# Optimization experiments

Hardware: AMD Instinct MI355X
Metric: run time of the kernel (lower is better)

Reference implementation:

```python
import jax, jax.numpy as jnp
import numpy as np

L, C, K, V, G, T, NC, CIN = 9, 256, 3, 25, 9, 128, 60, 3


def _ln(x, w, b, axes, eps=1e-5):
    # LayerNorm over (channels, joints) per time step, affine params broadcast over time
    m = x.mean(axes, keepdims=True)
    v = x.var(axes, keepdims=True)
    return (x - m) * jax.lax.rsqrt(v + eps) * w + b


def setup_inputs() -> dict:
    key = jax.random.key(0)
    ks = jax.random.split(key, 8)
    s = 0.02  # weight init scale
    return {
        "x": jax.random.normal(ks[0], (1, CIN, T, V), jnp.float32),
        "A": jax.random.uniform(ks[1], (K, V, V), jnp.float32),
        "ln_in_w": jnp.ones((CIN, V), jnp.float32),
        "ln_in_b": jnp.zeros((CIN, V), jnp.float32),
        "W_in": jax.random.normal(ks[2], (C, CIN), jnp.float32) * s,
        "b_in": jnp.zeros((C,), jnp.float32),
        "Wg": jax.random.normal(ks[3], (L, K * C, C), jnp.float32) * s,
        "bg": jnp.zeros((L, K * C), jnp.float32),
        "ln1_w": jnp.ones((L, C, V), jnp.float32),
        "ln1_b": jnp.zeros((L, C, V), jnp.float32),
        "Wt": jax.random.normal(ks[4], (L, C, C, G), jnp.float32) * s,
        "bt": jnp.zeros((L, C), jnp.float32),
        "ln2_w": jnp.ones((L, C, V), jnp.float32),
        "ln2_b": jnp.zeros((L, C, V), jnp.float32),
        "imp": jnp.ones((L, K, V, V), jnp.float32),
        "W_out": jax.random.normal(ks[5], (NC, C), jnp.float32) * s,
        "b_out": jnp.zeros((NC,), jnp.float32),
    }


def reference(x, A, ln_in_w, ln_in_b, W_in, b_in, Wg, bg, ln1_w, ln1_b,
              Wt, bt, ln2_w, ln2_b, imp, W_out, b_out):
    ghalf = G // 2
    Al = A[None] * imp                      # (L, K, V, V) edge-importance weighted adjacency
    xs = x[0].transpose(1, 0, 2)            # (T, CIN, V): stream frames
    fifo0 = jnp.zeros((L, C, G, V), x.dtype)

    def step(carry, xt):
        fifo, fifo_res = carry
        # input LayerNorm + 1x1 conv (fcn_in)
        h = _ln(xt, ln_in_w, ln_in_b, (0, 1))
        h = jnp.einsum('oc,cv->ov', W_in, h) + b_in[:, None]   # (C, V)
        new_f, new_fr = [], []
        for l in range(L):
            res = h                                             # identity residual (in==out, stride==1)
            # graph conv: 1x1 conv -> (K, C, V), einsum with partitioned adjacency
            y = (jnp.einsum('oc,cv->ov', Wg[l], h) + bg[l][:, None]).reshape(K, C, V)
            z = jnp.einsum('kcv,kvw->cw', y, Al[l])             # (C, V)
            # FIFO shift: newest frame at time index 0
            f = jnp.concatenate([z[:, None, :], fifo[l, :, :-1]], axis=1)      # (C, G, V)
            fr = jnp.concatenate([res[:, None, :], fifo_res[l, :, :-1]], axis=1)
            # tcn: LN -> ReLU -> temporal conv (G,1) -> LN
            a = jax.nn.relu(_ln(f, ln1_w[l][:, None, :], ln1_b[l][:, None, :], (0, 2)))
            t = jnp.einsum('ocg,cgv->ov', Wt[l], a) + bt[l][:, None]           # (C, V)
            t = _ln(t, ln2_w[l], ln2_b[l], (0, 1))
            # residual from center of residual FIFO, then ReLU
            h = jax.nn.relu(t + fr[:, ghalf])
            new_f.append(f)
            new_fr.append(fr)
        pooled = h.mean(axis=1)                                 # avg_pool2d over (T=1, V)
        logits = W_out @ pooled + b_out                         # (NC,)
        return (jnp.stack(new_f), jnp.stack(new_fr)), logits

    _, out = jax.lax.scan(step, (fifo0, fifo0), xs)
    return out  # (T, NC): per-frame class logits
```

## Files before the change

### kernel.cpp

```cpp
#include <hip/hip_runtime.h>

#define TT  128
#define CC  256
#define VV  25
#define KK  3
#define GG  9
#define LL  9
#define NCC 60
#define CINN 3
#define TV    (TT*VV)
#define N4    4096
#define KDIM2 (CC*GG)
#define UR    ((TT+8)*32)
#define YSTR  104
#define HSTR  264

typedef __attribute__((ext_vector_type(8))) short bf16x8;
typedef __attribute__((ext_vector_type(4))) float f32x4;
typedef unsigned short us16;

__device__ __forceinline__ us16 f2bf(float f) {
    union { float f; unsigned u; } a; a.f = f;
    unsigned r = a.u + 0x7fff + ((a.u >> 16) & 1);
    return (us16)(r >> 16);
}
__device__ __forceinline__ float bf2f(us16 u) {
    union { unsigned u; float f; } a; a.u = ((unsigned)u) << 16; return a.f;
}
__device__ __forceinline__ bf16x8 ld8(const us16* p) { return *(const bf16x8*)p; }


#define PN1 (LL*KK*CC*CC)
#define PN2 (LL*CC*CC*GG)
#define PN3 (LL*KK*32*32)
#define PN4 (LL*CC*32)
#define PTOT (PN1+PN2+PN3+PN4)

__global__ void k_prep(const float* __restrict__ Wg, const float* __restrict__ Wt,
                       const float* __restrict__ A, const float* __restrict__ imp,
                       const float* __restrict__ bg,
                       us16* __restrict__ Wgb, us16* __restrict__ Wt2b,
                       us16* __restrict__ AlTb, float* __restrict__ bgAl) {
    int i = blockIdx.x * 256 + threadIdx.x;
    if (i < PN1) {
        Wgb[i] = f2bf(Wg[i]);
    } else if (i < PN1 + PN2) {
        int j = i - PN1;
        int kk = j % (CC*GG);
        int o  = (j / (CC*GG)) % CC;
        int l  = j / (CC*CC*GG);
        int g = kk >> 8, c = kk & 255;
        Wt2b[j] = f2bf(Wt[((size_t)(l*CC + o)*CC + c)*GG + g]);
    } else if (i < PN1 + PN2 + PN3) {
        int j = i - PN1 - PN2;
        int v = j & 31, w = (j >> 5) & 31;
        int lk = j >> 10, k = lk % KK, l = lk / KK;
        float val = 0.f;
        if (v < VV && w < VV)
            val = A[(k*VV+v)*VV + w] * imp[((size_t)(l*KK+k)*VV+v)*VV + w];
        AlTb[j] = f2bf(val);
    } else if (i < PTOT) {
        int j = i - PN1 - PN2 - PN3;
        int w = j & 31, c = (j >> 5) & 255, l = j >> 13;
        float s = 0.f;
        if (w < VV) {
            for (int k = 0; k < KK; k++) {
                float col = 0.f;
                for (int v = 0; v < VV; v++)
                    col += A[(k*VV+v)*VV + w] * imp[((size_t)(l*KK+k)*VV+v)*VV + w];
                s += bg[l*KK*CC + k*CC + c] * col;
            }
        }
        bgAl[j] = s;
    }
}


__device__ __forceinline__ void blk_reduce2(float& s, float& q, float* red) {
    #pragma unroll
    for (int off = 32; off; off >>= 1) {
        s += __shfl_down(s, off);
        q += __shfl_down(q, off);
    }
    int lane = threadIdx.x & 63, w = threadIdx.x >> 6;
    if (lane == 0) { red[w] = s; red[4+w] = q; }
    __syncthreads();
    s = red[0]+red[1]+red[2]+red[3];
    q = red[4]+red[5]+red[6]+red[7];
}


template<int FIRST>
__global__ __launch_bounds__(256, 1) void k_gcn(
    const float* __restrict__ x, const float* __restrict__ lniw,
    const float* __restrict__ lnib, const float* __restrict__ Win,
    const float* __restrict__ bin,
    const us16* __restrict__ Tt, const float* __restrict__ btv,
    const float* __restrict__ ln2w, const float* __restrict__ ln2b,
    const us16* __restrict__ HresidTb,
    const us16* __restrict__ Wgb,
    const us16* __restrict__ AlTb, const float* __restrict__ bgAl,
    const float* __restrict__ lnw, const float* __restrict__ lnb,
    us16* __restrict__ HTb, us16* __restrict__ Ut2) {

    const int t = blockIdx.x, tid = threadIdx.x;
    if (t >= TT) {
        int tp = t - TT, c = tid;
        #pragma unroll
        for (int w = 0; w < 32; w++) {
            float u = (w < VV) ? fmaxf(lnb[c*VV + w], 0.f) : 0.f;
            Ut2[(size_t)(tp*32 + w)*CC + c] = f2bf(u);
        }
        return;
    }
    __shared__ __align__(16) us16 Yt[CC*YSTR];
    __shared__ __align__(16) us16 sH[32*HSTR];
    __shared__ float red[8];
    __shared__ float sx[80];
    __shared__ float sh[80];
    const int wave = tid >> 6, lane = tid & 63, quad = lane >> 4, l16 = lane & 15;

    if (FIRST) {
        if (tid < CINN*VV)
            sx[tid] = x[(size_t)(tid/VV)*TV + t*VV + (tid%VV)];
        __syncthreads();
        float s = 0.f, q = 0.f;
        for (int i = 0; i < CINN*VV; i++) { float v = sx[i]; s += v; q += v*v; }
        float m  = s * (1.f/75.f);
        float var = q * (1.f/75.f) - m*m;
        float rs = rsqrtf(var + 1e-5f);
        if (tid < CINN*VV)
            sh[tid] = (sx[tid]-m)*rs*lniw[tid] + lnib[tid];
        __syncthreads();
        int c = tid;
        float w0 = Win[c*3+0], w1 = Win[c*3+1], w2 = Win[c*3+2], bb = bin[c];
        #pragma unroll
        for (int v = 0; v < VV; v++) {
            float acc = bb + w0*sh[v] + w1*sh[VV+v] + w2*sh[2*VV+v];
            us16 b = f2bf(acc);
            HTb[(size_t)(t*32 + v)*CC + c] = b;
            sH[v*HSTR + c] = b;
        }
        #pragma unroll
        for (int v = VV; v < 32; v++)
            sH[v*HSTR + c] = 0;
        __syncthreads();
    } else {
        int c = tid;
        float btc = btv[c];
        float vals[VV];
        float s = 0.f, q = 0.f;
        #pragma unroll
        for (int v = 0; v < VV; v++) {
            float xv = bf2f(Tt[(size_t)(t*32 + v)*CC + c]) + btc;
            vals[v] = xv; s += xv; q += xv*xv;
        }
        blk_reduce2(s, q, red);
        float m = s * (1.f/6400.f);
        float var = q * (1.f/6400.f) - m*m;
        float rs = rsqrtf(var + 1e-5f);
        #pragma unroll
        for (int v = 0; v < VV; v++) {
            float res = (t >= 4) ? bf2f(HresidTb[(size_t)((t-4)*32 + v)*CC + c]) : 0.f;
            float o = fmaxf((vals[v]-m)*rs*ln2w[c*VV+v] + ln2b[c*VV+v] + res, 0.f);
            us16 b = f2bf(o);
            HTb[(size_t)(t*32 + v)*CC + c] = b;
            sH[v*HSTR + c] = b;
        }
        #pragma unroll
        for (int v = VV; v < 32; v++)
            sH[v*HSTR + c] = 0;
        __syncthreads();
    }

    bf16x8 al[2][3];
    #pragma unroll
    for (int nt = 0; nt < 2; nt++)
        #pragma unroll
        for (int s = 0; s < 3; s++)
            al[nt][s] = ld8(AlTb + (size_t)(s*32 + nt*16 + l16)*32 + quad*8);

    bf16x8 bf[2][8];
    #pragma unroll
    for (int nt = 0; nt < 2; nt++)
        #pragma unroll
        for (int s = 0; s < 8; s++)
            bf[nt][s] = *(const bf16x8*)(sH + (nt*16 + l16)*HSTR + s*32 + quad*8);

    bf16x8 wA0,wA1,wA2,wA3,wA4,wA5,wA6,wA7;
    bf16x8 wB0,wB1,wB2,wB3,wB4,wB5,wB6,wB7;
    bf16x8 wC0,wC1,wC2,wC3,wC4,wC5,wC6,wC7;

#define PLD(S, mtv) { \
    const us16* ap_ = Wgb + (size_t)(wave*192 + (mtv)*16 + l16)*CC + quad*8; \
    S##0 = ld8(ap_);       S##1 = ld8(ap_ + 32); \
    S##2 = ld8(ap_ + 64);  S##3 = ld8(ap_ + 96); \
    S##4 = ld8(ap_ + 128); S##5 = ld8(ap_ + 160); \
    S##6 = ld8(ap_ + 192); S##7 = ld8(ap_ + 224); }
#define PMFW(S, mtv) { \
    f32x4 p0a = {}, p0b = {}, p1a = {}, p1b = {}; \
    p0a = __builtin_amdgcn_mfma_f32_16x16x32_bf16(S##0, bf[0][0], p0a,0,0,0); \
    p1a = __builtin_amdgcn_mfma_f32_16x16x32_bf16(S##0, bf[1][0], p1a,0,0,0); \
    p0b = __builtin_amdgcn_mfma_f32_16x16x32_bf16(S##1, bf[0][1], p0b,0,0,0); \
    p1b = __builtin_amdgcn_mfma_f32_16x16x32_bf16(S##1, bf[1][1], p1b,0,0,0); \
    p0a = __builtin_amdgcn_mfma_f32_16x16x32_bf16(S##2, bf[0][2], p0a,0,0,0); \
    p1a = __builtin_amdgcn_mfma_f32_16x16x32_bf16(S##2, bf[1][2], p1a,0,0,0); \
    p0b = __builtin_amdgcn_mfma_f32_16x16x32_bf16(S##3, bf[0][3], p0b,0,0,0); \
    p1b = __builtin_amdgcn_mfma_f32_16x16x32_bf16(S##3, bf[1][3], p1b,0,0,0); \
    p0a = __builtin_amdgcn_mfma_f32_16x16x32_bf16(S##4, bf[0][4], p0a,0,0,0); \
    p1a = __builtin_amdgcn_mfma_f32_16x16x32_bf16(S##4, bf[1][4], p1a,0,0,0); \
    p0b = __builtin_amdgcn_mfma_f32_16x16x32_bf16(S##5, bf[0][5], p0b,0,0,0); \
    p1b = __builtin_amdgcn_mfma_f32_16x16x32_bf16(S##5, bf[1][5], p1b,0,0,0); \
    p0a = __builtin_amdgcn_mfma_f32_16x16x32_bf16(S##6, bf[0][6], p0a,0,0,0); \
    p1a = __builtin_amdgcn_mfma_f32_16x16x32_bf16(S##6, bf[1][6], p1a,0,0,0); \
    p0b = __builtin_amdgcn_mfma_f32_16x16x32_bf16(S##7, bf[0][7], p0b,0,0,0); \
    p1b = __builtin_amdgcn_mfma_f32_16x16x32_bf16(S##7, bf[1][7], p1b,0,0,0); \
    int mb_ = wave*192 + (mtv)*16 + quad*4; \
    _Pragma("unroll") \
    for (int r_ = 0; r_ < 4; r_++) { \
        int m_ = mb_ + r_; \
        int base_ = (m_ & 255)*YSTR + (m_ >> 8)*32 + l16; \
        Yt[base_]      = f2bf(p0a[r_] + p0b[r_]); \
        Yt[base_ + 16] = f2bf(p1a[r_] + p1b[r_]); \
    } }

    PLD(wA, 0); PLD(wB, 1); PLD(wC, 2);
    #pragma unroll 1
    for (int mt = 0; mt < 9; mt += 3) {
        PMFW(wA, mt);     PLD(wA, mt + 3);
        PMFW(wB, mt + 1); PLD(wB, mt + 4);
        PMFW(wC, mt + 2); PLD(wC, mt + 5);
    }
    PMFW(wA, 9); PMFW(wB, 10); PMFW(wC, 11);
#undef PLD
#undef PMFW
    __syncthreads();

    f32x4 z[4][2];
    #pragma unroll
    for (int mt = 0; mt < 4; mt++) { z[mt][0] = (f32x4){}; z[mt][1] = (f32x4){}; }
    #pragma unroll
    for (int mt = 0; mt < 4; mt++)
        #pragma unroll
        for (int s = 0; s < 3; s++) {
            bf16x8 a = *(const bf16x8*)(Yt + (wave*64 + mt*16 + l16)*YSTR + s*32 + quad*8);
            z[mt][0] = __builtin_amdgcn_mfma_f32_16x16x32_bf16(a, al[0][s], z[mt][0], 0,0,0);
            z[mt][1] = __builtin_amdgcn_mfma_f32_16x16x32_bf16(a, al[1][s], z[mt][1], 0,0,0);
        }

    float s_ = 0.f, q_ = 0.f;
    #pragma unroll
    for (int mt = 0; mt < 4; mt++)
        #pragma unroll
        for (int nt = 0; nt < 2; nt++)
            #pragma unroll
            for (int r = 0; r < 4; r++) {
                int c = wave*64 + mt*16 + quad*4 + r;
                int w = nt*16 + l16;
                float zb = z[mt][nt][r] + bgAl[c*32 + w];
                z[mt][nt][r] = zb;
                if (w < VV) { s_ += zb; q_ += zb*zb; }
            }
    blk_reduce2(s_, q_, red);
    float m = s_ * (1.f/6400.f);
    float var = q_ * (1.f/6400.f) - m*m;
    float rs = rsqrtf(var + 1e-5f);
    #pragma unroll
    for (int mt = 0; mt < 4; mt++)
        #pragma unroll
        for (int nt = 0; nt < 2; nt++) {
            int w = nt*16 + l16;
            if (w < VV) {
                int c0 = wave*64 + mt*16 + quad*4;
                ushort4 pk;
                float u0 = fmaxf((z[mt][nt][0]-m)*rs*lnw[(c0+0)*VV+w] + lnb[(c0+0)*VV+w], 0.f);
                float u1 = fmaxf((z[mt][nt][1]-m)*rs*lnw[(c0+1)*VV+w] + lnb[(c0+1)*VV+w], 0.f);
                float u2 = fmaxf((z[mt][nt][2]-m)*rs*lnw[(c0+2)*VV+w] + lnb[(c0+2)*VV+w], 0.f);
                float u3 = fmaxf((z[mt][nt][3]-m)*rs*lnw[(c0+3)*VV+w] + lnb[(c0+3)*VV+w], 0.f);
                pk.x = f2bf(u0); pk.y = f2bf(u1); pk.z = f2bf(u2); pk.w = f2bf(u3);
                *(ushort4*)(Ut2 + (size_t)((t+8)*32 + w)*CC + c0) = pk;
            }
        }
    #pragma unroll
    for (int r = VV; r < 32; r++)
        Ut2[(size_t)((t+8)*32 + r)*CC + tid] = 0;
}


__global__ __launch_bounds__(256) void k_gemm2(const us16* __restrict__ A,
                                               const us16* __restrict__ Ut2,
                                               us16* __restrict__ Tt) {
    __shared__ us16 TL[64*72];
    const int tid = threadIdx.x;
    const int wave = tid >> 6, lane = tid & 63, quad = lane >> 4, l16 = lane & 15;
    const int bid = blockIdx.x;
    const int xcd = bid & 7, grp = bid >> 3;
    const int mt = (xcd >> 2)*2 + (grp & 1);
    const int nt = (xcd & 3)*16 + (grp >> 1);
    const int m0b = mt*64, n0b = nt*64;
    const int m0w = m0b + (wave & 1)*32;
    const int n0w = n0b + (wave >> 1)*32;
    const us16* ap = A + (size_t)(m0w + l16)*KDIM2 + quad*8;
    f32x4 acc00 = {}, acc01 = {}, acc10 = {}, acc11 = {};
    bf16x8 aA0,aA1,bA0,bA1, aB0,aB1,bB0,bB1, aC0,aC1,bC0,bC1, aD0,aD1,bD0,bD1;

#define GLD(S, it) { \
    int k0 = (it)*32; \
    a##S##0 = ld8(ap + k0); \
    a##S##1 = ld8(ap + k0 + 16*KDIM2); \
    int g = k0 >> 8; \
    const us16* bp = Ut2 + (size_t)(n0w + (8-g)*32 + l16)*CC + (k0 & 255) + quad*8; \
    b##S##0 = ld8(bp); \
    b##S##1 = ld8(bp + 16*CC); }
#define GMF(S) { \
    acc00 = __builtin_amdgcn_mfma_f32_16x16x32_bf16(a##S##0, b##S##0, acc00,0,0,0); \
    acc01 = __builtin_amdgcn_mfma_f32_16x16x32_bf16(a##S##0, b##S##1, acc01,0,0,0); \
    acc10 = __builtin_amdgcn_mfma_f32_16x16x32_bf16(a##S##1, b##S##0, acc10,0,0,0); \
    acc11 = __builtin_amdgcn_mfma_f32_16x16x32_bf16(a##S##1, b##S##1, acc11,0,0,0); }

    GLD(A, 0); GLD(B, 1); GLD(C, 2); GLD(D, 3);
    #pragma unroll 1
    for (int it = 4; it <= KDIM2/32 - 4; it += 4) {
        GMF(A); GLD(A, it);
        GMF(B); GLD(B, it+1);
        GMF(C); GLD(C, it+2);
        GMF(D); GLD(D, it+3);
    }
    GMF(A); GMF(B); GMF(C); GMF(D);
#undef GLD
#undef GMF

    #pragma unroll
    for (int r = 0; r < 4; r++) {
        int mlo = (wave & 1)*32 + quad*4 + r;
        int nlo = (wave >> 1)*32 + l16;
        TL[nlo*72 + mlo]           = f2bf(acc00[r]);
        TL[(nlo+16)*72 + mlo]      = f2bf(acc01[r]);
        TL[nlo*72 + mlo + 16]      = f2bf(acc10[r]);
        TL[(nlo+16)*72 + mlo + 16] = f2bf(acc11[r]);
    }
    __syncthreads();
    #pragma unroll
    for (int u = 0; u < 2; u++) {
        int q2 = tid + u*256;
        int row = q2 >> 3, ch = q2 & 7;
        *(bf16x8*)(Tt + (size_t)(n0b + row)*CC + m0b + ch*8) =
            *(const bf16x8*)(TL + row*72 + ch*8);
    }
}


__global__ __launch_bounds__(256) void k_fin(const us16* __restrict__ Tt,
                                             const us16* __restrict__ HresidTb,
                                             const float* __restrict__ btv,
                                             const float* __restrict__ lnw,
                                             const float* __restrict__ lnb,
                                             const float* __restrict__ Wout,
                                             const float* __restrict__ bout,
                                             float* __restrict__ out) {
    int t = blockIdx.x, tid = threadIdx.x;
    __shared__ float red[8];
    __shared__ float sp[CC];
    int c = tid;
    float btc = btv[c];
    float vals[VV];
    float s = 0.f, q = 0.f;
    #pragma unroll
    for (int v = 0; v < VV; v++) {
        float xv = bf2f(Tt[(size_t)(t*32 + v)*CC + c]) + btc;
        vals[v] = xv; s += xv; q += xv*xv;
    }
    blk_reduce2(s, q, red);
    float m = s * (1.f/6400.f);
    float var = q * (1.f/6400.f) - m*m;
    float rs = rsqrtf(var + 1e-5f);
    float pl = 0.f;
    #pragma unroll
    for (int v = 0; v < VV; v++) {
        float res = (t >= 4) ? bf2f(HresidTb[(size_t)((t-4)*32 + v)*CC + c]) : 0.f;
        float o = fmaxf((vals[v]-m)*rs*lnw[c*VV+v] + lnb[c*VV+v] + res, 0.f);
        pl += o;
    }
    sp[c] = pl * (1.f/VV);
    __syncthreads();
    if (tid < NCC) {
        float a = bout[tid];
        for (int cc = 0; cc < CC; cc++) a = fmaf(Wout[tid*CC+cc], sp[cc], a);
        out[t*NCC + tid] = a;
    }
}


extern "C" void kernel_launch(void* const* d_in, const int* in_sizes, int n_in,
                              void* d_out, int out_size, void* d_ws, size_t ws_size,
                              hipStream_t stream) {
    const float* x    = (const float*)d_in[0];
    const float* A    = (const float*)d_in[1];
    const float* lniw = (const float*)d_in[2];
    const float* lnib = (const float*)d_in[3];
    const float* Win  = (const float*)d_in[4];
    const float* bin  = (const float*)d_in[5];
    const float* Wg   = (const float*)d_in[6];
    const float* bg   = (const float*)d_in[7];
    const float* ln1w = (const float*)d_in[8];
    const float* ln1b = (const float*)d_in[9];
    const float* Wt   = (const float*)d_in[10];
    const float* bt   = (const float*)d_in[11];
    const float* ln2w = (const float*)d_in[12];
    const float* ln2b = (const float*)d_in[13];
    const float* imp  = (const float*)d_in[14];
    const float* Wout = (const float*)d_in[15];
    const float* bout = (const float*)d_in[16];
    float* out = (float*)d_out;

    float* ws = (float*)d_ws;
    size_t off = 0;
    auto alloc = [&](size_t n) { float* p = ws + off; off += (n + 255) & ~(size_t)255; return p; };
    float* bgAl = alloc((size_t)LL*CC*32);
    us16* HTb0 = (us16*)alloc((size_t)TT*32*CC/2);
    us16* HTb1 = (us16*)alloc((size_t)TT*32*CC/2);
    us16* Tt   = (us16*)alloc((size_t)N4*CC/2);
    us16* Wgb  = (us16*)alloc((size_t)LL*KK*CC*CC/2);
    us16* Wt2b = (us16*)alloc((size_t)LL*CC*KDIM2/2);
    us16* Ut2  = (us16*)alloc((size_t)UR*CC/2);
    us16* AlTb = (us16*)alloc((size_t)LL*KK*32*32/2);
    (void)ws_size; (void)in_sizes; (void)n_in; (void)out_size;

    k_prep<<<(PTOT + 255)/256, 256, 0, stream>>>(Wg, Wt, A, imp, bg,
                                                 Wgb, Wt2b, AlTb, bgAl);

    us16* hPrev = HTb0; us16* hNext = HTb1;
    for (int l = 0; l < LL; l++) {
        if (l == 0) {
            k_gcn<1><<<TT + 8, 256, 0, stream>>>(
                x, lniw, lnib, Win, bin,
                Tt, bt, ln2w, ln2b, hPrev,
                Wgb, AlTb, bgAl, ln1w, ln1b,
                hPrev , Ut2);
        } else {
            k_gcn<0><<<TT + 8, 256, 0, stream>>>(
                x, lniw, lnib, Win, bin,
                Tt, bt + (size_t)(l-1)*CC,
                ln2w + (size_t)(l-1)*CC*VV, ln2b + (size_t)(l-1)*CC*VV,
                hPrev ,
                Wgb + (size_t)l*KK*CC*CC,
                AlTb + (size_t)l*KK*32*32, bgAl + (size_t)l*CC*32,
                ln1w + (size_t)l*CC*VV, ln1b + (size_t)l*CC*VV,
                hNext , Ut2);
            us16* tmp = hPrev; hPrev = hNext; hNext = tmp;
        }
        k_gemm2<<<256, 256, 0, stream>>>(
            Wt2b + (size_t)l*CC*KDIM2, Ut2, Tt);
    }
    k_fin<<<TT, 256, 0, stream>>>(Tt, hPrev,
        bt + (size_t)(LL-1)*CC, ln2w + (size_t)(LL-1)*CC*VV, ln2b + (size_t)(LL-1)*CC*VV,
        Wout, bout, out);
}
```

Measured before the change: 712.5 us.

## Split temporal-conv GEMM K dimension in two with fp32 partial outputs

The temporal-conv GEMM is split along its K dimension (2304) into two halves of 36 iterations each, doubling the grid from 256 to 512 blocks. Each half writes fp32 partial sums to its own buffer, and the consumer kernels (k_gcn and k_fin) add the two partials when they read them. The aim is better occupancy of the GPU's compute units with twice as many blocks, each running a shorter K loop. In exchange, the intermediate buffer grows fourfold (two fp32 copies instead of one bf16 copy), which adds write and read traffic, and each block's pipeline prologue and epilogue is amortised over fewer iterations.

```diff
diff --git a/kernel.cpp b/kernel.cpp
--- a/kernel.cpp
+++ b/kernel.cpp
@@ -95,7 +95,7 @@
     const float* __restrict__ x, const float* __restrict__ lniw,
     const float* __restrict__ lnib, const float* __restrict__ Win,
     const float* __restrict__ bin,
-    const us16* __restrict__ Tt, const float* __restrict__ btv,
+    const float* __restrict__ Tp, const float* __restrict__ btv,
     const float* __restrict__ ln2w, const float* __restrict__ ln2b,
     const us16* __restrict__ HresidTb,
     const us16* __restrict__ Wgb,
@@ -152,7 +152,8 @@
         float s = 0.f, q = 0.f;
         #pragma unroll
         for (int v = 0; v < VV; v++) {
-            float xv = bf2f(Tt[(size_t)(t*32 + v)*CC + c]) + btc;
+            size_t idx = (size_t)(t*32 + v)*CC + c;
+            float xv = Tp[idx] + Tp[(size_t)N4*CC + idx] + btc;
             vals[v] = xv; s += xv; q += xv*xv;
         }
         blk_reduce2(s, q, red);
@@ -289,17 +290,19 @@
 
 __global__ __launch_bounds__(256) void k_gemm2(const us16* __restrict__ A,
                                                const us16* __restrict__ Ut2,
-                                               us16* __restrict__ Tt) {
-    __shared__ us16 TL[64*72];
+                                               float* __restrict__ Tp) {
+    __shared__ __align__(16) float TLf[64*72];
     const int tid = threadIdx.x;
     const int wave = tid >> 6, lane = tid & 63, quad = lane >> 4, l16 = lane & 15;
     const int bid = blockIdx.x;
-    const int xcd = bid & 7, grp = bid >> 3;
+    const int inner = bid & 255, ks = bid >> 8;
+    const int xcd = inner & 7, grp = inner >> 3;
     const int mt = (xcd >> 2)*2 + (grp & 1);
     const int nt = (xcd & 3)*16 + (grp >> 1);
     const int m0b = mt*64, n0b = nt*64;
     const int m0w = m0b + (wave & 1)*32;
     const int n0w = n0b + (wave >> 1)*32;
+    const int it0 = ks*36;
     const us16* ap = A + (size_t)(m0w + l16)*KDIM2 + quad*8;
     f32x4 acc00 = {}, acc01 = {}, acc10 = {}, acc11 = {};
     bf16x8 aA0,aA1,bA0,bA1, aB0,aB1,bB0,bB1, aC0,aC1,bC0,bC1, aD0,aD1,bD0,bD1;
@@ -318,9 +321,9 @@
     acc10 = __builtin_amdgcn_mfma_f32_16x16x32_bf16(a##S##1, b##S##0, acc10,0,0,0); \
     acc11 = __builtin_amdgcn_mfma_f32_16x16x32_bf16(a##S##1, b##S##1, acc11,0,0,0); }
 
-    GLD(A, 0); GLD(B, 1); GLD(C, 2); GLD(D, 3);
+    GLD(A, it0); GLD(B, it0+1); GLD(C, it0+2); GLD(D, it0+3);
     #pragma unroll 1
-    for (int it = 4; it <= KDIM2/32 - 4; it += 4) {
+    for (int it = it0 + 4; it <= it0 + 36 - 4; it += 4) {
         GMF(A); GLD(A, it);
         GMF(B); GLD(B, it+1);
         GMF(C); GLD(C, it+2);
@@ -334,23 +337,24 @@
     for (int r = 0; r < 4; r++) {
         int mlo = (wave & 1)*32 + quad*4 + r;
         int nlo = (wave >> 1)*32 + l16;
-        TL[nlo*72 + mlo]           = f2bf(acc00[r]);
-        TL[(nlo+16)*72 + mlo]      = f2bf(acc01[r]);
-        TL[nlo*72 + mlo + 16]      = f2bf(acc10[r]);
-        TL[(nlo+16)*72 + mlo + 16] = f2bf(acc11[r]);
+        TLf[nlo*72 + mlo]           = acc00[r];
+        TLf[(nlo+16)*72 + mlo]      = acc01[r];
+        TLf[nlo*72 + mlo + 16]      = acc10[r];
+        TLf[(nlo+16)*72 + mlo + 16] = acc11[r];
     }
     __syncthreads();
-    #pragma unroll
-    for (int u = 0; u < 2; u++) {
+    float* dst = Tp + (size_t)ks*N4*CC;
+    #pragma unroll
+    for (int u = 0; u < 4; u++) {
         int q2 = tid + u*256;
-        int row = q2 >> 3, ch = q2 & 7;
-        *(bf16x8*)(Tt + (size_t)(n0b + row)*CC + m0b + ch*8) =
-            *(const bf16x8*)(TL + row*72 + ch*8);
-    }
-}
-
-
-__global__ __launch_bounds__(256) void k_fin(const us16* __restrict__ Tt,
+        int row = q2 >> 4, ch = q2 & 15;
+        *(float4*)(dst + (size_t)(n0b + row)*CC + m0b + ch*4) =
+            *(const float4*)(TLf + row*72 + ch*4);
+    }
+}
+
+
+__global__ __launch_bounds__(256) void k_fin(const float* __restrict__ Tp,
                                              const us16* __restrict__ HresidTb,
                                              const float* __restrict__ btv,
                                              const float* __restrict__ lnw,
@@ -367,7 +371,8 @@
     float s = 0.f, q = 0.f;
     #pragma unroll
     for (int v = 0; v < VV; v++) {
-        float xv = bf2f(Tt[(size_t)(t*32 + v)*CC + c]) + btc;
+        size_t idx = (size_t)(t*32 + v)*CC + c;
+        float xv = Tp[idx] + Tp[(size_t)N4*CC + idx] + btc;
         vals[v] = xv; s += xv; q += xv*xv;
     }
     blk_reduce2(s, q, red);
@@ -419,7 +424,7 @@
     float* bgAl = alloc((size_t)LL*CC*32);
     us16* HTb0 = (us16*)alloc((size_t)TT*32*CC/2);
     us16* HTb1 = (us16*)alloc((size_t)TT*32*CC/2);
-    us16* Tt   = (us16*)alloc((size_t)N4*CC/2);
+    float* Tp  = alloc((size_t)2*N4*CC);
     us16* Wgb  = (us16*)alloc((size_t)LL*KK*CC*CC/2);
     us16* Wt2b = (us16*)alloc((size_t)LL*CC*KDIM2/2);
     us16* Ut2  = (us16*)alloc((size_t)UR*CC/2);
@@ -434,13 +439,13 @@
         if (l == 0) {
             k_gcn<1><<<TT + 8, 256, 0, stream>>>(
                 x, lniw, lnib, Win, bin,
-                Tt, bt, ln2w, ln2b, hPrev,
+                Tp, bt, ln2w, ln2b, hPrev,
                 Wgb, AlTb, bgAl, ln1w, ln1b,
                 hPrev , Ut2);
         } else {
             k_gcn<0><<<TT + 8, 256, 0, stream>>>(
                 x, lniw, lnib, Win, bin,
-                Tt, bt + (size_t)(l-1)*CC,
+                Tp, bt + (size_t)(l-1)*CC,
                 ln2w + (size_t)(l-1)*CC*VV, ln2b + (size_t)(l-1)*CC*VV,
                 hPrev ,
                 Wgb + (size_t)l*KK*CC*CC,
@@ -449,10 +454,10 @@
                 hNext , Ut2);
             us16* tmp = hPrev; hPrev = hNext; hNext = tmp;
         }
-        k_gemm2<<<256, 256, 0, stream>>>(
-            Wt2b + (size_t)l*CC*KDIM2, Ut2, Tt);
-    }
-    k_fin<<<TT, 256, 0, stream>>>(Tt, hPrev,
+        k_gemm2<<<512, 256, 0, stream>>>(
+            Wt2b + (size_t)l*CC*KDIM2, Ut2, Tp);
+    }
+    k_fin<<<TT, 256, 0, stream>>>(Tp, hPrev,
         bt + (size_t)(LL-1)*CC, ln2w + (size_t)(LL-1)*CC*VV, ln2b + (size_t)(LL-1)*CC*VV,
         Wout, bout, out);
 }
```

After: 734.3 us. 1.03x slower.

## Fuse per-layer kernels into one persistent kernel with grid barriers

Applied to the files above, without the earlier changes.

Replaces the 19 separate launches (graph-conv kernel and temporal GEMM per layer, plus the final head) with one persistent 256-block kernel. Stages are separated by a software grid barrier built on device-scope atomics, and the barrier counter is zeroed in the prep kernel. This removes launch overhead and the gaps between kernels. In exchange, all 256 blocks must be co-resident, the barrier spin costs time, and the ping-pong pointer swap happens before the barrier. Register and LDS pressure also rise, since both stages now share one kernel.

```diff
diff --git a/kernel.cpp b/kernel.cpp
--- a/kernel.cpp
+++ b/kernel.cpp
@@ -14,6 +14,7 @@
 #define UR    ((TT+8)*32)
 #define YSTR  104
 #define HSTR  264
+#define GRID  256
 
 typedef __attribute__((ext_vector_type(8))) short bf16x8;
 typedef __attribute__((ext_vector_type(4))) float f32x4;
@@ -28,6 +29,25 @@
     union { unsigned u; float f; } a; a.u = ((unsigned)u) << 16; return a.f;
 }
 __device__ __forceinline__ bf16x8 ld8(const us16* p) { return *(const bf16x8*)p; }
+
+
+__device__ __forceinline__ void gbar(unsigned* bar) {
+    __syncthreads();
+    if (threadIdx.x == 0) {
+        __threadfence();
+        unsigned g = __hip_atomic_load(bar + 1, __ATOMIC_RELAXED, __HIP_MEMORY_SCOPE_AGENT);
+        unsigned a = __hip_atomic_fetch_add(bar, 1u, __ATOMIC_ACQ_REL, __HIP_MEMORY_SCOPE_AGENT);
+        if (a == GRID - 1) {
+            __hip_atomic_store(bar, 0u, __ATOMIC_RELAXED, __HIP_MEMORY_SCOPE_AGENT);
+            __hip_atomic_store(bar + 1, g + 1u, __ATOMIC_RELEASE, __HIP_MEMORY_SCOPE_AGENT);
+        } else {
+            while (__hip_atomic_load(bar + 1, __ATOMIC_ACQUIRE, __HIP_MEMORY_SCOPE_AGENT) == g)
+                __builtin_amdgcn_s_sleep(2);
+        }
+        __threadfence();
+    }
+    __syncthreads();
+}
 
 
 #define PN1 (LL*KK*CC*CC)
@@ -40,8 +60,10 @@
                        const float* __restrict__ A, const float* __restrict__ imp,
                        const float* __restrict__ bg,
                        us16* __restrict__ Wgb, us16* __restrict__ Wt2b,
-                       us16* __restrict__ AlTb, float* __restrict__ bgAl) {
+                       us16* __restrict__ AlTb, float* __restrict__ bgAl,
+                       unsigned* __restrict__ bar) {
     int i = blockIdx.x * 256 + threadIdx.x;
+    if (i < 8) bar[i] = 0u;
     if (i < PN1) {
         Wgb[i] = f2bf(Wg[i]);
     } else if (i < PN1 + PN2) {
@@ -90,109 +112,124 @@
 }
 
 
-template<int FIRST>
-__global__ __launch_bounds__(256, 1) void k_gcn(
-    const float* __restrict__ x, const float* __restrict__ lniw,
-    const float* __restrict__ lnib, const float* __restrict__ Win,
-    const float* __restrict__ bin,
-    const us16* __restrict__ Tt, const float* __restrict__ btv,
-    const float* __restrict__ ln2w, const float* __restrict__ ln2b,
-    const us16* __restrict__ HresidTb,
-    const us16* __restrict__ Wgb,
-    const us16* __restrict__ AlTb, const float* __restrict__ bgAl,
-    const float* __restrict__ lnw, const float* __restrict__ lnb,
-    us16* __restrict__ HTb, us16* __restrict__ Ut2) {
-
-    const int t = blockIdx.x, tid = threadIdx.x;
-    if (t >= TT) {
-        int tp = t - TT, c = tid;
-        #pragma unroll
-        for (int w = 0; w < 32; w++) {
-            float u = (w < VV) ? fmaxf(lnb[c*VV + w], 0.f) : 0.f;
-            Ut2[(size_t)(tp*32 + w)*CC + c] = f2bf(u);
-        }
-        return;
-    }
+struct FA {
+    const float *x, *lniw, *lnib, *Win, *bin;
+    const float *bt, *ln2w, *ln2b;
+    const float *ln1w, *ln1b;
+    const us16  *Wgb, *AlTb, *Wt2b;
+    const float *bgAl;
+    const float *Wout, *bout;
+    us16 *HTb0, *HTb1, *Tt, *Ut2;
+    unsigned *bar;
+    float *out;
+};
+
+__global__ __launch_bounds__(256, 1) void k_fused(FA a) {
+    const int bid = blockIdx.x, tid = threadIdx.x;
     __shared__ __align__(16) us16 Yt[CC*YSTR];
     __shared__ __align__(16) us16 sH[32*HSTR];
     __shared__ float red[8];
     __shared__ float sx[80];
     __shared__ float sh[80];
     const int wave = tid >> 6, lane = tid & 63, quad = lane >> 4, l16 = lane & 15;
-
-    if (FIRST) {
-        if (tid < CINN*VV)
-            sx[tid] = x[(size_t)(tid/VV)*TV + t*VV + (tid%VV)];
-        __syncthreads();
-        float s = 0.f, q = 0.f;
-        for (int i = 0; i < CINN*VV; i++) { float v = sx[i]; s += v; q += v*v; }
-        float m  = s * (1.f/75.f);
-        float var = q * (1.f/75.f) - m*m;
-        float rs = rsqrtf(var + 1e-5f);
-        if (tid < CINN*VV)
-            sh[tid] = (sx[tid]-m)*rs*lniw[tid] + lnib[tid];
-        __syncthreads();
-        int c = tid;
-        float w0 = Win[c*3+0], w1 = Win[c*3+1], w2 = Win[c*3+2], bb = bin[c];
-        #pragma unroll
-        for (int v = 0; v < VV; v++) {
-            float acc = bb + w0*sh[v] + w1*sh[VV+v] + w2*sh[2*VV+v];
-            us16 b = f2bf(acc);
-            HTb[(size_t)(t*32 + v)*CC + c] = b;
-            sH[v*HSTR + c] = b;
-        }
-        #pragma unroll
-        for (int v = VV; v < 32; v++)
-            sH[v*HSTR + c] = 0;
-        __syncthreads();
-    } else {
-        int c = tid;
-        float btc = btv[c];
-        float vals[VV];
-        float s = 0.f, q = 0.f;
-        #pragma unroll
-        for (int v = 0; v < VV; v++) {
-            float xv = bf2f(Tt[(size_t)(t*32 + v)*CC + c]) + btc;
-            vals[v] = xv; s += xv; q += xv*xv;
-        }
-        blk_reduce2(s, q, red);
-        float m = s * (1.f/6400.f);
-        float var = q * (1.f/6400.f) - m*m;
-        float rs = rsqrtf(var + 1e-5f);
-        #pragma unroll
-        for (int v = 0; v < VV; v++) {
-            float res = (t >= 4) ? bf2f(HresidTb[(size_t)((t-4)*32 + v)*CC + c]) : 0.f;
-            float o = fmaxf((vals[v]-m)*rs*ln2w[c*VV+v] + ln2b[c*VV+v] + res, 0.f);
-            us16 b = f2bf(o);
-            HTb[(size_t)(t*32 + v)*CC + c] = b;
-            sH[v*HSTR + c] = b;
-        }
-        #pragma unroll
-        for (int v = VV; v < 32; v++)
-            sH[v*HSTR + c] = 0;
-        __syncthreads();
-    }
-
-    bf16x8 al[2][3];
-    #pragma unroll
-    for (int nt = 0; nt < 2; nt++)
-        #pragma unroll
-        for (int s = 0; s < 3; s++)
-            al[nt][s] = ld8(AlTb + (size_t)(s*32 + nt*16 + l16)*32 + quad*8);
-
-    bf16x8 bf[2][8];
-    #pragma unroll
-    for (int nt = 0; nt < 2; nt++)
-        #pragma unroll
-        for (int s = 0; s < 8; s++)
-            bf[nt][s] = *(const bf16x8*)(sH + (nt*16 + l16)*HSTR + s*32 + quad*8);
-
-    bf16x8 wA0,wA1,wA2,wA3,wA4,wA5,wA6,wA7;
-    bf16x8 wB0,wB1,wB2,wB3,wB4,wB5,wB6,wB7;
-    bf16x8 wC0,wC1,wC2,wC3,wC4,wC5,wC6,wC7;
+    const int t = bid;
+
+    us16* hPrev = a.HTb0;
+    us16* hNext = a.HTb1;
+
+    #pragma unroll 1
+    for (int l = 0; l < LL; l++) {
+        const us16*  WgbL  = a.Wgb  + (size_t)l*KK*CC*CC;
+        const us16*  AlTbL = a.AlTb + (size_t)l*KK*32*32;
+        const float* bgAlL = a.bgAl + (size_t)l*CC*32;
+        const float* lnwL  = a.ln1w + (size_t)l*CC*VV;
+        const float* lnbL  = a.ln1b + (size_t)l*CC*VV;
+        us16* Hout = (l == 0) ? hPrev : hNext;
+
+        if (t >= TT && t < TT + 8) {
+            int tp = t - TT, c = tid;
+            #pragma unroll
+            for (int w = 0; w < 32; w++) {
+                float u = (w < VV) ? fmaxf(lnbL[c*VV + w], 0.f) : 0.f;
+                a.Ut2[(size_t)(tp*32 + w)*CC + c] = f2bf(u);
+            }
+        } else if (t < TT) {
+            if (l == 0) {
+                if (tid < CINN*VV)
+                    sx[tid] = a.x[(size_t)(tid/VV)*TV + t*VV + (tid%VV)];
+                __syncthreads();
+                float s = 0.f, q = 0.f;
+                for (int i = 0; i < CINN*VV; i++) { float v = sx[i]; s += v; q += v*v; }
+                float m  = s * (1.f/75.f);
+                float var = q * (1.f/75.f) - m*m;
+                float rs = rsqrtf(var + 1e-5f);
+                if (tid < CINN*VV)
+                    sh[tid] = (sx[tid]-m)*rs*a.lniw[tid] + a.lnib[tid];
+                __syncthreads();
+                int c = tid;
+                float w0 = a.Win[c*3+0], w1 = a.Win[c*3+1], w2 = a.Win[c*3+2], bb = a.bin[c];
+                #pragma unroll
+                for (int v = 0; v < VV; v++) {
+                    float acc = bb + w0*sh[v] + w1*sh[VV+v] + w2*sh[2*VV+v];
+                    us16 b = f2bf(acc);
+                    Hout[(size_t)(t*32 + v)*CC + c] = b;
+                    sH[v*HSTR + c] = b;
+                }
+                #pragma unroll
+                for (int v = VV; v < 32; v++)
+                    sH[v*HSTR + c] = 0;
+                __syncthreads();
+            } else {
+                const float* btv = a.bt   + (size_t)(l-1)*CC;
+                const float* l2w = a.ln2w + (size_t)(l-1)*CC*VV;
+                const float* l2b = a.ln2b + (size_t)(l-1)*CC*VV;
+                int c = tid;
+                float btc = btv[c];
+                float vals[VV];
+                float s = 0.f, q = 0.f;
+                #pragma unroll
+                for (int v = 0; v < VV; v++) {
+                    float xv = bf2f(a.Tt[(size_t)(t*32 + v)*CC + c]) + btc;
+                    vals[v] = xv; s += xv; q += xv*xv;
+                }
+                blk_reduce2(s, q, red);
+                float m = s * (1.f/6400.f);
+                float var = q * (1.f/6400.f) - m*m;
+                float rs = rsqrtf(var + 1e-5f);
+                #pragma unroll
+                for (int v = 0; v < VV; v++) {
+                    float res = (t >= 4) ? bf2f(hPrev[(size_t)((t-4)*32 + v)*CC + c]) : 0.f;
+                    float o = fmaxf((vals[v]-m)*rs*l2w[c*VV+v] + l2b[c*VV+v] + res, 0.f);
+                    us16 b = f2bf(o);
+                    Hout[(size_t)(t*32 + v)*CC + c] = b;
+                    sH[v*HSTR + c] = b;
+                }
+                #pragma unroll
+                for (int v = VV; v < 32; v++)
+                    sH[v*HSTR + c] = 0;
+                __syncthreads();
+            }
+
+            bf16x8 al[2][3];
+            #pragma unroll
+            for (int nt = 0; nt < 2; nt++)
+                #pragma unroll
+                for (int s = 0; s < 3; s++)
+                    al[nt][s] = ld8(AlTbL + (size_t)(s*32 + nt*16 + l16)*32 + quad*8);
+
+            bf16x8 bf[2][8];
+            #pragma unroll
+            for (int nt = 0; nt < 2; nt++)
+                #pragma unroll
+                for (int s = 0; s < 8; s++)
+                    bf[nt][s] = *(const bf16x8*)(sH + (nt*16 + l16)*HSTR + s*32 + quad*8);
+
+            bf16x8 wA0,wA1,wA2,wA3,wA4,wA5,wA6,wA7;
+            bf16x8 wB0,wB1,wB2,wB3,wB4,wB5,wB6,wB7;
+            bf16x8 wC0,wC1,wC2,wC3,wC4,wC5,wC6,wC7;
 
 #define PLD(S, mtv) { \
-    const us16* ap_ = Wgb + (size_t)(wave*192 + (mtv)*16 + l16)*CC + quad*8; \
+    const us16* ap_ = WgbL + (size_t)(wave*192 + (mtv)*16 + l16)*CC + quad*8; \
     S##0 = ld8(ap_);       S##1 = ld8(ap_ + 32); \
     S##2 = ld8(ap_ + 64);  S##3 = ld8(ap_ + 96); \
     S##4 = ld8(ap_ + 128); S##5 = ld8(ap_ + 160); \
@@ -224,92 +261,90 @@
         Yt[base_ + 16] = f2bf(p1a[r_] + p1b[r_]); \
     } }
 
-    PLD(wA, 0); PLD(wB, 1); PLD(wC, 2);
-    #pragma unroll 1
-    for (int mt = 0; mt < 9; mt += 3) {
-        PMFW(wA, mt);     PLD(wA, mt + 3);
-        PMFW(wB, mt + 1); PLD(wB, mt + 4);
-        PMFW(wC, mt + 2); PLD(wC, mt + 5);
-    }
-    PMFW(wA, 9); PMFW(wB, 10); PMFW(wC, 11);
+            PLD(wA, 0); PLD(wB, 1); PLD(wC, 2);
+            #pragma unroll 1
+            for (int mt = 0; mt < 9; mt += 3) {
+                PMFW(wA, mt);     PLD(wA, mt + 3);
+                PMFW(wB, mt + 1); PLD(wB, mt + 4);
+                PMFW(wC, mt + 2); PLD(wC, mt + 5);
+            }
+            PMFW(wA, 9); PMFW(wB, 10); PMFW(wC, 11);
 #undef PLD
 #undef PMFW
-    __syncthreads();
-
-    f32x4 z[4][2];
-    #pragma unroll
-    for (int mt = 0; mt < 4; mt++) { z[mt][0] = (f32x4){}; z[mt][1] = (f32x4){}; }
-    #pragma unroll
-    for (int mt = 0; mt < 4; mt++)
-        #pragma unroll
-        for (int s = 0; s < 3; s++) {
-            bf16x8 a = *(const bf16x8*)(Yt + (wave*64 + mt*16 + l16)*YSTR + s*32 + quad*8);
-            z[mt][0] = __builtin_amdgcn_mfma_f32_16x16x32_bf16(a, al[0][s], z[mt][0], 0,0,0);
-            z[mt][1] = __builtin_amdgcn_mfma_f32_16x16x32_bf16(a, al[1][s], z[mt][1], 0,0,0);
-        }
-
-    float s_ = 0.f, q_ = 0.f;
-    #pragma unroll
-    for (int mt = 0; mt < 4; mt++)
-        #pragma unroll
-        for (int nt = 0; nt < 2; nt++)
-            #pragma unroll
-            for (int r = 0; r < 4; r++) {
-                int c = wave*64 + mt*16 + quad*4 + r;
-                int w = nt*16 + l16;
-                float zb = z[mt][nt][r] + bgAl[c*32 + w];
-                z[mt][nt][r] = zb;
-                if (w < VV) { s_ += zb; q_ += zb*zb; }
-            }
-    blk_reduce2(s_, q_, red);
-    float m = s_ * (1.f/6400.f);
-    float var = q_ * (1.f/6400.f) - m*m;
-    float rs = rsqrtf(var + 1e-5f);
-    #pragma unroll
-    for (int mt = 0; mt < 4; mt++)
-        #pragma unroll
-        for (int nt = 0; nt < 2; nt++) {
-            int w = nt*16 + l16;
-            if (w < VV) {
-                int c0 = wave*64 + mt*16 + quad*4;
-                ushort4 pk;
-                float u0 = fmaxf((z[mt][nt][0]-m)*rs*lnw[(c0+0)*VV+w] + lnb[(c0+0)*VV+w], 0.f);
-                float u1 = fmaxf((z[mt][nt][1]-m)*rs*lnw[(c0+1)*VV+w] + lnb[(c0+1)*VV+w], 0.f);
-                float u2 = fmaxf((z[mt][nt][2]-m)*rs*lnw[(c0+2)*VV+w] + lnb[(c0+2)*VV+w], 0.f);
-                float u3 = fmaxf((z[mt][nt][3]-m)*rs*lnw[(c0+3)*VV+w] + lnb[(c0+3)*VV+w], 0.f);
-                pk.x = f2bf(u0); pk.y = f2bf(u1); pk.z = f2bf(u2); pk.w = f2bf(u3);
-                *(ushort4*)(Ut2 + (size_t)((t+8)*32 + w)*CC + c0) = pk;
-            }
-        }
-    #pragma unroll
-    for (int r = VV; r < 32; r++)
-        Ut2[(size_t)((t+8)*32 + r)*CC + tid] = 0;
-}
-
-
-__global__ __launch_bounds__(256) void k_gemm2(const us16* __restrict__ A,
-                                               const us16* __restrict__ Ut2,
-                                               us16* __restrict__ Tt) {
-    __shared__ us16 TL[64*72];
-    const int tid = threadIdx.x;
-    const int wave = tid >> 6, lane = tid & 63, quad = lane >> 4, l16 = lane & 15;
-    const int bid = blockIdx.x;
-    const int xcd = bid & 7, grp = bid >> 3;
-    const int mt = (xcd >> 2)*2 + (grp & 1);
-    const int nt = (xcd & 3)*16 + (grp >> 1);
-    const int m0b = mt*64, n0b = nt*64;
-    const int m0w = m0b + (wave & 1)*32;
-    const int n0w = n0b + (wave >> 1)*32;
-    const us16* ap = A + (size_t)(m0w + l16)*KDIM2 + quad*8;
-    f32x4 acc00 = {}, acc01 = {}, acc10 = {}, acc11 = {};
-    bf16x8 aA0,aA1,bA0,bA1, aB0,aB1,bB0,bB1, aC0,aC1,bC0,bC1, aD0,aD1,bD0,bD1;
+            __syncthreads();
+
+            f32x4 z[4][2];
+            #pragma unroll
+            for (int mt = 0; mt < 4; mt++) { z[mt][0] = (f32x4){}; z[mt][1] = (f32x4){}; }
+            #pragma unroll
+            for (int mt = 0; mt < 4; mt++)
+                #pragma unroll
+                for (int s = 0; s < 3; s++) {
+                    bf16x8 av = *(const bf16x8*)(Yt + (wave*64 + mt*16 + l16)*YSTR + s*32 + quad*8);
+                    z[mt][0] = __builtin_amdgcn_mfma_f32_16x16x32_bf16(av, al[0][s], z[mt][0], 0,0,0);
+                    z[mt][1] = __builtin_amdgcn_mfma_f32_16x16x32_bf16(av, al[1][s], z[mt][1], 0,0,0);
+                }
+
+            float s_ = 0.f, q_ = 0.f;
+            #pragma unroll
+            for (int mt = 0; mt < 4; mt++)
+                #pragma unroll
+                for (int nt = 0; nt < 2; nt++)
+                    #pragma unroll
+                    for (int r = 0; r < 4; r++) {
+                        int c = wave*64 + mt*16 + quad*4 + r;
+                        int w = nt*16 + l16;
+                        float zb = z[mt][nt][r] + bgAlL[c*32 + w];
+                        z[mt][nt][r] = zb;
+                        if (w < VV) { s_ += zb; q_ += zb*zb; }
+                    }
+            blk_reduce2(s_, q_, red);
+            float m = s_ * (1.f/6400.f);
+            float var = q_ * (1.f/6400.f) - m*m;
+            float rs = rsqrtf(var + 1e-5f);
+            #pragma unroll
+            for (int mt = 0; mt < 4; mt++)
+                #pragma unroll
+                for (int nt = 0; nt < 2; nt++) {
+                    int w = nt*16 + l16;
+                    if (w < VV) {
+                        int c0 = wave*64 + mt*16 + quad*4;
+                        ushort4 pk;
+                        float u0 = fmaxf((z[mt][nt][0]-m)*rs*lnwL[(c0+0)*VV+w] + lnbL[(c0+0)*VV+w], 0.f);
+                        float u1 = fmaxf((z[mt][nt][1]-m)*rs*lnwL[(c0+1)*VV+w] + lnbL[(c0+1)*VV+w], 0.f);
+                        float u2 = fmaxf((z[mt][nt][2]-m)*rs*lnwL[(c0+2)*VV+w] + lnbL[(c0+2)*VV+w], 0.f);
+                        float u3 = fmaxf((z[mt][nt][3]-m)*rs*lnwL[(c0+3)*VV+w] + lnbL[(c0+3)*VV+w], 0.f);
+                        pk.x = f2bf(u0); pk.y = f2bf(u1); pk.z = f2bf(u2); pk.w = f2bf(u3);
+                        *(ushort4*)(a.Ut2 + (size_t)((t+8)*32 + w)*CC + c0) = pk;
+                    }
+                }
+            #pragma unroll
+            for (int r = VV; r < 32; r++)
+                a.Ut2[(size_t)((t+8)*32 + r)*CC + tid] = 0;
+        }
+
+        if (l > 0) { us16* tmp = hPrev; hPrev = hNext; hNext = tmp; }
+        gbar(a.bar);
+
+        {
+            const us16* Awt = a.Wt2b + (size_t)l*CC*KDIM2;
+            us16* TL = Yt;
+            const int xcd = bid & 7, grp = bid >> 3;
+            const int mt = (xcd >> 2)*2 + (grp & 1);
+            const int nt = (xcd & 3)*16 + (grp >> 1);
+            const int m0b = mt*64, n0b = nt*64;
+            const int m0w = m0b + (wave & 1)*32;
+            const int n0w = n0b + (wave >> 1)*32;
+            const us16* ap = Awt + (size_t)(m0w + l16)*KDIM2 + quad*8;
+            f32x4 acc00 = {}, acc01 = {}, acc10 = {}, acc11 = {};
+            bf16x8 aA0,aA1,bA0,bA1, aB0,aB1,bB0,bB1, aC0,aC1,bC0,bC1, aD0,aD1,bD0,bD1;
 
 #define GLD(S, it) { \
     int k0 = (it)*32; \
     a##S##0 = ld8(ap + k0); \
     a##S##1 = ld8(ap + k0 + 16*KDIM2); \
     int g = k0 >> 8; \
-    const us16* bp = Ut2 + (size_t)(n0w + (8-g)*32 + l16)*CC + (k0 & 255) + quad*8; \
+    const us16* bp = a.Ut2 + (size_t)(n0w + (8-g)*32 + l16)*CC + (k0 & 255) + quad*8; \
     b##S##0 = ld8(bp); \
     b##S##1 = ld8(bp + 16*CC); }
 #define GMF(S) { \
@@ -318,75 +353,71 @@
     acc10 = __builtin_amdgcn_mfma_f32_16x16x32_bf16(a##S##1, b##S##0, acc10,0,0,0); \
     acc11 = __builtin_amdgcn_mfma_f32_16x16x32_bf16(a##S##1, b##S##1, acc11,0,0,0); }
 
-    GLD(A, 0); GLD(B, 1); GLD(C, 2); GLD(D, 3);
-    #pragma unroll 1
-    for (int it = 4; it <= KDIM2/32 - 4; it += 4) {
-        GMF(A); GLD(A, it);
-        GMF(B); GLD(B, it+1);
-        GMF(C); GLD(C, it+2);
-        GMF(D); GLD(D, it+3);
-    }
-    GMF(A); GMF(B); GMF(C); GMF(D);
+            GLD(A, 0); GLD(B, 1); GLD(C, 2); GLD(D, 3);
+            #pragma unroll 1
+            for (int it = 4; it <= KDIM2/32 - 4; it += 4) {
+                GMF(A); GLD(A, it);
+                GMF(B); GLD(B, it+1);
+                GMF(C); GLD(C, it+2);
+                GMF(D); GLD(D, it+3);
+            }
+            GMF(A); GMF(B); GMF(C); GMF(D);
 #undef GLD
 #undef GMF
 
-    #pragma unroll
-    for (int r = 0; r < 4; r++) {
-        int mlo = (wave & 1)*32 + quad*4 + r;
-        int nlo = (wave >> 1)*32 + l16;
-        TL[nlo*72 + mlo]           = f2bf(acc00[r]);
-        TL[(nlo+16)*72 + mlo]      = f2bf(acc01[r]);
-        TL[nlo*72 + mlo + 16]      = f2bf(acc10[r]);
-        TL[(nlo+16)*72 + mlo + 16] = f2bf(acc11[r]);
+            #pragma unroll
+            for (int r = 0; r < 4; r++) {
+                int mlo = (wave & 1)*32 + quad*4 + r;
+                int nlo = (wave >> 1)*32 + l16;
+                TL[nlo*72 + mlo]           = f2bf(acc00[r]);
+                TL[(nlo+16)*72 + mlo]      = f2bf(acc01[r]);
+                TL[nlo*72 + mlo + 16]      = f2bf(acc10[r]);
+                TL[(nlo+16)*72 + mlo + 16] = f2bf(acc11[r]);
+            }
+            __syncthreads();
+            #pragma unroll
+            for (int u = 0; u < 2; u++) {
+                int q2 = tid + u*256;
+                int row = q2 >> 3, ch = q2 & 7;
+                *(bf16x8*)(a.Tt + (size_t)(n0b + row)*CC + m0b + ch*8) =
+                    *(const bf16x8*)(TL + row*72 + ch*8);
+            }
+        }
+        gbar(a.bar);
     }
-    __syncthreads();
-    #pragma unroll
-    for (int u = 0; u < 2; u++) {
-        int q2 = tid + u*256;
-        int row = q2 >> 3, ch = q2 & 7;
-        *(bf16x8*)(Tt + (size_t)(n0b + row)*CC + m0b + ch*8) =
-            *(const bf16x8*)(TL + row*72 + ch*8);
-    }
-}
-
-
-__global__ __launch_bounds__(256) void k_fin(const us16* __restrict__ Tt,
-                                             const us16* __restrict__ HresidTb,
-                                             const float* __restrict__ btv,
-                                             const float* __restrict__ lnw,
-                                             const float* __restrict__ lnb,
-                                             const float* __restrict__ Wout,
-                                             const float* __restrict__ bout,
-                                             float* __restrict__ out) {
-    int t = blockIdx.x, tid = threadIdx.x;
-    __shared__ float red[8];
-    __shared__ float sp[CC];
-    int c = tid;
-    float btc = btv[c];
-    float vals[VV];
-    float s = 0.f, q = 0.f;
-    #pragma unroll
-    for (int v = 0; v < VV; v++) {
-        float xv = bf2f(Tt[(size_t)(t*32 + v)*CC + c]) + btc;
-        vals[v] = xv; s += xv; q += xv*xv;
-    }
-    blk_reduce2(s, q, red);
-    float m = s * (1.f/6400.f);
-    float var = q * (1.f/6400.f) - m*m;
-    float rs = rsqrtf(var + 1e-5f);
-    float pl = 0.f;
-    #pragma unroll
-    for (int v = 0; v < VV; v++) {
-        float res = (t >= 4) ? bf2f(HresidTb[(size_t)((t-4)*32 + v)*CC + c]) : 0.f;
-        float o = fmaxf((vals[v]-m)*rs*lnw[c*VV+v] + lnb[c*VV+v] + res, 0.f);
-        pl += o;
-    }
-    sp[c] = pl * (1.f/VV);
-    __syncthreads();
-    if (tid < NCC) {
-        float a = bout[tid];
-        for (int cc = 0; cc < CC; cc++) a = fmaf(Wout[tid*CC+cc], sp[cc], a);
-        out[t*NCC + tid] = a;
+
+    if (t < TT) {
+        const float* btv = a.bt   + (size_t)(LL-1)*CC;
+        const float* lnw = a.ln2w + (size_t)(LL-1)*CC*VV;
+        const float* lnb = a.ln2b + (size_t)(LL-1)*CC*VV;
+        float* sp = (float*)sH;
+        int c = tid;
+        float btc = btv[c];
+        float vals[VV];
+        float s = 0.f, q = 0.f;
+        #pragma unroll
+        for (int v = 0; v < VV; v++) {
+            float xv = bf2f(a.Tt[(size_t)(t*32 + v)*CC + c]) + btc;
+            vals[v] = xv; s += xv; q += xv*xv;
+        }
+        blk_reduce2(s, q, red);
+        float m = s * (1.f/6400.f);
+        float var = q * (1.f/6400.f) - m*m;
+        float rs = rsqrtf(var + 1e-5f);
+        float pl = 0.f;
+        #pragma unroll
+        for (int v = 0; v < VV; v++) {
+            float res = (t >= 4) ? bf2f(hPrev[(size_t)((t-4)*32 + v)*CC + c]) : 0.f;
+            float o = fmaxf((vals[v]-m)*rs*lnw[c*VV+v] + lnb[c*VV+v] + res, 0.f);
+            pl += o;
+        }
+        sp[c] = pl * (1.f/VV);
+        __syncthreads();
+        if (tid < NCC) {
+            float acc = a.bout[tid];
+            for (int cc = 0; cc < CC; cc++) acc = fmaf(a.Wout[tid*CC+cc], sp[cc], acc);
+            a.out[t*NCC + tid] = acc;
+        }
     }
 }
 
@@ -424,35 +455,22 @@
     us16* Wt2b = (us16*)alloc((size_t)LL*CC*KDIM2/2);
     us16* Ut2  = (us16*)alloc((size_t)UR*CC/2);
     us16* AlTb = (us16*)alloc((size_t)LL*KK*32*32/2);
+    unsigned* bar = (unsigned*)alloc(256);
     (void)ws_size; (void)in_sizes; (void)n_in; (void)out_size;
 
     k_prep<<<(PTOT + 255)/256, 256, 0, stream>>>(Wg, Wt, A, imp, bg,
-                                                 Wgb, Wt2b, AlTb, bgAl);
-
-    us16* hPrev = HTb0; us16* hNext = HTb1;
-    for (int l = 0; l < LL; l++) {
-        if (l == 0) {
-            k_gcn<1><<<TT + 8, 256, 0, stream>>>(
-                x, lniw, lnib, Win, bin,
-                Tt, bt, ln2w, ln2b, hPrev,
-                Wgb, AlTb, bgAl, ln1w, ln1b,
-                hPrev , Ut2);
-        } else {
-            k_gcn<0><<<TT + 8, 256, 0, stream>>>(
-                x, lniw, lnib, Win, bin,
-                Tt, bt + (size_t)(l-1)*CC,
-                ln2w + (size_t)(l-1)*CC*VV, ln2b + (size_t)(l-1)*CC*VV,
-                hPrev ,
-                Wgb + (size_t)l*KK*CC*CC,
-                AlTb + (size_t)l*KK*32*32, bgAl + (size_t)l*CC*32,
-                ln1w + (size_t)l*CC*VV, ln1b + (size_t)l*CC*VV,
-                hNext , Ut2);
-            us16* tmp = hPrev; hPrev = hNext; hNext = tmp;
-        }
-        k_gemm2<<<256, 256, 0, stream>>>(
-            Wt2b + (size_t)l*CC*KDIM2, Ut2, Tt);
-    }
-    k_fin<<<TT, 256, 0, stream>>>(Tt, hPrev,
-        bt + (size_t)(LL-1)*CC, ln2w + (size_t)(LL-1)*CC*VV, ln2b + (size_t)(LL-1)*CC*VV,
-        Wout, bout, out);
-}
+                                                 Wgb, Wt2b, AlTb, bgAl, bar);
+
+    FA fa;
+    fa.x = x; fa.lniw = lniw; fa.lnib = lnib; fa.Win = Win; fa.bin = bin;
+    fa.bt = bt; fa.ln2w = ln2w; fa.ln2b = ln2b;
+    fa.ln1w = ln1w; fa.ln1b = ln1b;
+    fa.Wgb = Wgb; fa.AlTb = AlTb; fa.Wt2b = Wt2b;
+    fa.bgAl = bgAl;
+    fa.Wout = Wout; fa.bout = bout;
+    fa.HTb0 = HTb0; fa.HTb1 = HTb1; fa.Tt = Tt; fa.Ut2 = Ut2;
+    fa.bar = bar;
+    fa.out = out;
+
+    k_fused<<<dim3(GRID), dim3(256), 0, stream>>>(fa);
+}
```

New measurement: 2.441 ms. 3.43x slower.
